# Kernel tuning notes

Measured on AMD Instinct MI355X. Metric: run time of the kernel, lower is better.

The kernel has to match this reference:

```python
import jax, jax.numpy as jnp
import numpy as np

H = 16  # num heads

def setup_inputs() -> dict:
    key = jax.random.key(0)
    ks = jax.random.split(key, 5)
    B, S, D = 4, 2048, 1024
    scale = 1.0 / np.sqrt(D)
    return {
        "hidden_states": jax.random.normal(ks[0], (B, S, D), dtype=jnp.float32),
        "Wq": jax.random.normal(ks[1], (D, D), dtype=jnp.float32) * scale,
        "Wk": jax.random.normal(ks[2], (D, D), dtype=jnp.float32) * scale,
        "Wv": jax.random.normal(ks[3], (D, D), dtype=jnp.float32) * scale,
        "Wo": jax.random.normal(ks[4], (D, D), dtype=jnp.float32) * scale,
    }

def reference(hidden_states, Wq, Wk, Wv, Wo):
    B, S, D = hidden_states.shape
    hd = D // H  # attention_head_size

    def split_heads(x):  # [B,S,D] -> [B,H,S,hd]
        return x.reshape(B, S, H, hd).transpose(0, 2, 1, 3)

    # torch Linear (no bias): y = x @ W.T
    q = split_heads(hidden_states @ Wq.T)
    k = split_heads(hidden_states @ Wk.T)
    v = split_heads(hidden_states @ Wv.T)

    scores = jnp.einsum('bhqd,bhkd->bhqk', q, k) / jnp.sqrt(jnp.float32(hd))
    probs = jax.nn.softmax(scores, axis=-1)  # dropout p=0 -> identity
    ctx = jnp.einsum('bhqk,bhkd->bhqd', probs, v)
    ctx = ctx.transpose(0, 2, 1, 3).reshape(B, S, D)
    out = ctx @ Wo.T
    return out
```

## Files before the change

### kernel.cpp

```cpp
#include <hip/hip_runtime.h>

typedef _Float16 half8 __attribute__((ext_vector_type(8)));
typedef _Float16 half4 __attribute__((ext_vector_type(4)));
typedef float f32x4 __attribute__((ext_vector_type(4)));

#define GLOAD16(gptr, lptr)                                                               \
  __builtin_amdgcn_global_load_lds((const __attribute__((address_space(1))) void*)(gptr), \
                                   (__attribute__((address_space(3))) void*)(lptr), 16, 0, 0)

#define MEMFENCE asm volatile("" ::: "memory")

constexpr int B_ = 4, S_ = 2048, D_ = 1024;
constexpr int M_ = B_ * S_;

__global__ __launch_bounds__(256) void cvt_all(
    const float* __restrict__ x, const float* __restrict__ wq,
    const float* __restrict__ wk, const float* __restrict__ wv,
    const float* __restrict__ wo, _Float16* __restrict__ xb,
    _Float16* __restrict__ wb ) {
  int bx = blockIdx.x;
  const float* src;
  _Float16* dst;
  long i;
  if (bx < 4096) {
    src = x; dst = xb; i = (long)bx * 256 + threadIdx.x;
  } else {
    int seg = (bx - 4096) >> 9;
    src = seg == 0 ? wq : seg == 1 ? wk : seg == 2 ? wv : wo;
    dst = wb + (long)seg * D_ * D_;
    i = (long)((bx - 4096) & 511) * 256 + threadIdx.x;
  }
  const float4* s4 = (const float4*)src;
  float4 a = s4[2 * i], b = s4[2 * i + 1];
  half8 o = {(_Float16)a.x, (_Float16)a.y, (_Float16)a.z, (_Float16)a.w,
             (_Float16)b.x, (_Float16)b.y, (_Float16)b.z, (_Float16)b.w};
  *(half8*)(dst + 8 * i) = o;
}

__device__ __forceinline__ void gemm_core(const _Float16* __restrict__ A,
                                          const _Float16* __restrict__ W,
                                          _Float16* As, _Float16* Bs, long m0,
                                          long n0, int t, f32x4 acc[4][4]) {
  const int lane = t & 63, w = t >> 6, wr = w >> 1, wc = w & 1;
  const int r16 = lane & 15, g = lane >> 4;
  const int srow = t >> 2, schunk = t & 3;
  const int sc = schunk ^ (srow & 3);
  const _Float16* Ap = A + (m0 + srow) * D_ + sc * 8;
  const _Float16* Wp = W + (n0 + srow) * D_ + sc * 8;
  _Float16* Ad = As + srow * 32 + schunk * 8;
  _Float16* Bd = Bs + srow * 32 + schunk * 8;
  for (int k0 = 0; k0 < D_; k0 += 32) {
    GLOAD16(Ap + k0, Ad);
    GLOAD16(Ap + 64 * D_ + k0, Ad + 64 * 32);
    GLOAD16(Wp + k0, Bd);
    GLOAD16(Wp + 64 * D_ + k0, Bd + 64 * 32);
    __syncthreads();
    half8 af[4], bf[4];
#pragma unroll
    for (int i = 0; i < 4; ++i) {
      int ra = wr * 64 + i * 16 + r16;
      int rb = wc * 64 + i * 16 + r16;
      af[i] = *(const half8*)(As + ra * 32 + ((g ^ (ra & 3)) * 8));
      bf[i] = *(const half8*)(Bs + rb * 32 + ((g ^ (rb & 3)) * 8));
    }
#pragma unroll
    for (int i = 0; i < 4; ++i)
#pragma unroll
      for (int j = 0; j < 4; ++j)
        acc[i][j] =
            __builtin_amdgcn_mfma_f32_16x16x32_f16(af[i], bf[j], acc[i][j], 0, 0, 0);
    __syncthreads();
  }
}

__global__ __launch_bounds__(256, 2) void gemm_qkv(
    const _Float16* __restrict__ A, const _Float16* __restrict__ Wq,
    const _Float16* __restrict__ Wk, const _Float16* __restrict__ Wv,
    _Float16* __restrict__ Qo, _Float16* __restrict__ Ko,
    _Float16* __restrict__ Vt) {
  __shared__ _Float16 As[128 * 32], Bs[128 * 32];
  const int t = threadIdx.x;
  const int sel = blockIdx.y >> 3;
  const _Float16* W = sel == 0 ? Wq : (sel == 1 ? Wk : Wv);
  long m0 = (long)blockIdx.x * 128;
  long n0 = (long)(blockIdx.y & 7) * 128;
  f32x4 acc[4][4] = {};
  gemm_core(A, W, As, Bs, m0, n0, t, acc);
  const int lane = t & 63, w = t >> 6, wr = w >> 1, wc = w & 1;
  const int r16 = lane & 15, g = lane >> 4;
  if (sel < 2) {
    _Float16* C = sel == 0 ? Qo : Ko;
#pragma unroll
    for (int i = 0; i < 4; ++i)
#pragma unroll
      for (int j = 0; j < 4; ++j)
#pragma unroll
        for (int r = 0; r < 4; ++r) {
          long mr = m0 + wr * 64 + i * 16 + g * 4 + r;
          long nc = n0 + wc * 64 + j * 16 + r16;
          C[mr * D_ + nc] = (_Float16)acc[i][j][r];
        }
  } else {
#pragma unroll
    for (int i = 0; i < 4; ++i)
#pragma unroll
      for (int j = 0; j < 4; ++j)
#pragma unroll
        for (int r = 0; r < 4; ++r) {
          long mr = m0 + wr * 64 + i * 16 + g * 4 + r;
          long nc = n0 + wc * 64 + j * 16 + r16;
          long bb = mr >> 11, ss = mr & 2047;
          long hh = nc >> 6, dd = nc & 63;
          Vt[(((bb * 16 + hh) * 64 + dd) << 11) + ss] = (_Float16)acc[i][j][r];
        }
  }
}

__global__ __launch_bounds__(256, 2) void gemm_out(const _Float16* __restrict__ A,
                                                   const _Float16* __restrict__ W,
                                                   float* __restrict__ C) {
  __shared__ _Float16 As[128 * 32], Bs[128 * 32];
  const int t = threadIdx.x;
  long m0 = (long)blockIdx.x * 128;
  long n0 = (long)blockIdx.y * 128;
  f32x4 acc[4][4] = {};
  gemm_core(A, W, As, Bs, m0, n0, t, acc);
  const int lane = t & 63, w = t >> 6, wr = w >> 1, wc = w & 1;
  const int r16 = lane & 15, g = lane >> 4;
#pragma unroll
  for (int i = 0; i < 4; ++i)
#pragma unroll
    for (int j = 0; j < 4; ++j)
#pragma unroll
      for (int r = 0; r < 4; ++r) {
        long mr = m0 + wr * 64 + i * 16 + g * 4 + r;
        long nc = n0 + wc * 64 + j * 16 + r16;
        C[mr * D_ + nc] = acc[i][j][r];
      }
}

__global__ __launch_bounds__(512, 4) void attn_kernel(
    const _Float16* __restrict__ Q, const _Float16* __restrict__ K,
    const _Float16* __restrict__ Vt, _Float16* __restrict__ Ctx) {
  __shared__ _Float16 Ks[2][64 * 64], Vs[2][64 * 64];
  const int t = threadIdx.x, lane = t & 63, w = t >> 6;
  const int r16 = lane & 15, g = lane >> 4;
  const int q0 = blockIdx.x * 256;
  const int bh = blockIdx.y;
  const int b = bh >> 4, h = bh & 15;
  const long qkbase = ((long)b * S_) * D_ + h * 64;
  const long vtbase = (long)bh * 64 * S_;

  half8 qf[2][2];
#pragma unroll
  for (int mi = 0; mi < 2; ++mi)
#pragma unroll
    for (int ks = 0; ks < 2; ++ks) {
      int row = q0 + w * 32 + mi * 16 + r16;
      half8 v = *(const half8*)(Q + qkbase + (long)row * D_ + ks * 32 + g * 8);
      qf[mi][ks] = v * (_Float16)0.125f;
    }
  asm volatile("s_waitcnt vmcnt(0)" ::: "memory");

  f32x4 ctx[2][4] = {};
  float lsum[2] = {0.f, 0.f};

  const int srowt = t >> 3, schunk = t & 7;
  const int sc = schunk ^ (srowt & 7);
  const _Float16* Kg = K + qkbase + (long)srowt * D_ + sc * 8;
  const _Float16* Vg = Vt + vtbase + (long)srowt * S_ + sc * 8;

#define STAGE(kt, buf)                                                  \
  do {                                                                  \
    GLOAD16(Kg + (long)(kt)*64 * D_, &Ks[buf][srowt * 64 + schunk * 8]); \
    GLOAD16(Vg + (kt)*64, &Vs[buf][srowt * 64 + schunk * 8]);            \
  } while (0)

  STAGE(0, 0);
  constexpr int NT = S_ / 64;
  for (int kt = 0; kt < NT; ++kt) {
    const int cur = kt & 1;
    if (kt + 1 < NT) {
      STAGE(kt + 1, cur ^ 1);
      asm volatile("s_waitcnt vmcnt(2)" ::: "memory");
    } else {
      asm volatile("s_waitcnt vmcnt(0)" ::: "memory");
    }
    __builtin_amdgcn_s_barrier();
    MEMFENCE;
    __builtin_amdgcn_sched_barrier(0);
    const _Float16* Kc = Ks[cur];
    const _Float16* Vc = Vs[cur];

    f32x4 sf[4][2] = {};
#pragma unroll
    for (int kn = 0; kn < 4; ++kn) {
#pragma unroll
      for (int ks = 0; ks < 2; ++ks) {
        int row = kn * 16 + r16;
        int ch = ks * 4 + g;
        half8 kf = *(const half8*)(Kc + row * 64 + ((ch ^ (row & 7)) * 8));
        sf[kn][0] = __builtin_amdgcn_mfma_f32_16x16x32_f16(kf, qf[0][ks], sf[kn][0], 0, 0, 0);
        sf[kn][1] = __builtin_amdgcn_mfma_f32_16x16x32_f16(kf, qf[1][ks], sf[kn][1], 0, 0, 0);
      }
    }

    half4 pt[4][2];
#pragma unroll
    for (int kn = 0; kn < 4; ++kn)
#pragma unroll
      for (int mi = 0; mi < 2; ++mi) {
        float p0 = __expf(sf[kn][mi][0]);
        float p1 = __expf(sf[kn][mi][1]);
        float p2 = __expf(sf[kn][mi][2]);
        float p3 = __expf(sf[kn][mi][3]);
        lsum[mi] += (p0 + p1) + (p2 + p3);
        half4 pk = {(_Float16)p0, (_Float16)p1, (_Float16)p2, (_Float16)p3};
        pt[kn][mi] = pk;
      }

#pragma unroll
    for (int ni = 0; ni < 4; ++ni) {
      int row = ni * 16 + r16;
#pragma unroll
      for (int kt16 = 0; kt16 < 4; ++kt16) {
        int ch = kt16 * 2 + (g >> 1);
        half4 vf = *(const half4*)(Vc + row * 64 + ((ch ^ (row & 7)) * 8) + (g & 1) * 4);
        ctx[0][ni] = __builtin_amdgcn_mfma_f32_16x16x16f16(pt[kt16][0], vf, ctx[0][ni], 0, 0, 0);
        ctx[1][ni] = __builtin_amdgcn_mfma_f32_16x16x16f16(pt[kt16][1], vf, ctx[1][ni], 0, 0, 0);
      }
    }
    __builtin_amdgcn_sched_barrier(0);
    asm volatile("s_waitcnt lgkmcnt(0)" ::: "memory");
    MEMFENCE;
    __builtin_amdgcn_s_barrier();
    MEMFENCE;
  }
#undef STAGE

  float linv[2];
#pragma unroll
  for (int mi = 0; mi < 2; ++mi) {
    float v = lsum[mi];
    v += __shfl_xor(v, 16);
    v += __shfl_xor(v, 32);
    linv[mi] = 1.f / v;
  }
#pragma unroll
  for (int mi = 0; mi < 2; ++mi)
#pragma unroll
    for (int r = 0; r < 4; ++r) {
      float inv = __shfl(linv[mi], g * 4 + r, 16);
      long qrow = (long)b * S_ + q0 + w * 32 + mi * 16 + g * 4 + r;
#pragma unroll
      for (int ni = 0; ni < 4; ++ni)
        Ctx[qrow * D_ + h * 64 + ni * 16 + r16] = (_Float16)(ctx[mi][ni][r] * inv);
    }
}

extern "C" void kernel_launch(void* const* d_in, const int* in_sizes, int n_in,
                              void* d_out, int out_size, void* d_ws, size_t ws_size,
                              hipStream_t stream) {
  (void)in_sizes; (void)n_in; (void)out_size; (void)ws_size;
  const float* x = (const float*)d_in[0];
  const float* Wq = (const float*)d_in[1];
  const float* Wk = (const float*)d_in[2];
  const float* Wv = (const float*)d_in[3];
  const float* Wo = (const float*)d_in[4];
  char* ws = (char*)d_ws;
  _Float16* xb = (_Float16*)ws;
  _Float16* wb = (_Float16*)(ws + (size_t)16 * 1024 * 1024);
  _Float16* wqb = wb;
  _Float16* wkb = wb + (size_t)D_ * D_;
  _Float16* wvb = wb + (size_t)2 * D_ * D_;
  _Float16* wob = wb + (size_t)3 * D_ * D_;
  _Float16* qb = (_Float16*)(ws + (size_t)24 * 1024 * 1024);
  _Float16* kb = qb + (size_t)M_ * D_;
  _Float16* vtb = kb + (size_t)M_ * D_;
  _Float16* ctxb = vtb + (size_t)M_ * D_;

  cvt_all<<<4096 + 4 * 512, 256, 0, stream>>>(x, Wq, Wk, Wv, Wo, xb, wb);
  gemm_qkv<<<dim3(64, 24), 256, 0, stream>>>(xb, wqb, wkb, wvb, qb, kb, vtb);
  attn_kernel<<<dim3(8, 64), 512, 0, stream>>>(qb, kb, vtb, ctxb);
  gemm_out<<<dim3(64, 8), 256, 0, stream>>>(ctxb, wob, (float*)d_out);
}
```

Baseline: 202.0 us.

## Fold softmax scale and log2e into Q projection, permute Vt for 16-byte LDS reads

The 1/sqrt(hd)·log2(e) factor is now applied in the QKV GEMM epilogue, so the attention kernel drops its per-fragment Q multiply and calls exp2f instead of __expf. The V-transpose store permutes the sequence index within each 64-block so the PV loop can load one half8 per LDS read and split it into two half4 MFMA operands, halving the number of LDS reads for V. This saves exp-argument scaling and LDS instructions in the inner loop, at the cost of extra index arithmetic in the V store epilogue and a layout the two kernels must agree on.

```diff
diff --git a/kernel.cpp b/kernel.cpp
--- a/kernel.cpp
+++ b/kernel.cpp
@@ -12,6 +12,7 @@
 
 constexpr int B_ = 4, S_ = 2048, D_ = 1024;
 constexpr int M_ = B_ * S_;
+#define QSCALE 0.18033688f
 
 __global__ __launch_bounds__(256) void cvt_all(
     const float* __restrict__ x, const float* __restrict__ wq,
@@ -90,6 +91,7 @@
   const int r16 = lane & 15, g = lane >> 4;
   if (sel < 2) {
     _Float16* C = sel == 0 ? Qo : Ko;
+    const float qs = sel == 0 ? QSCALE : 1.0f;
 #pragma unroll
     for (int i = 0; i < 4; ++i)
 #pragma unroll
@@ -98,7 +100,7 @@
         for (int r = 0; r < 4; ++r) {
           long mr = m0 + wr * 64 + i * 16 + g * 4 + r;
           long nc = n0 + wc * 64 + j * 16 + r16;
-          C[mr * D_ + nc] = (_Float16)acc[i][j][r];
+          C[mr * D_ + nc] = (_Float16)(acc[i][j][r] * qs);
         }
   } else {
 #pragma unroll
@@ -110,8 +112,11 @@
           long mr = m0 + wr * 64 + i * 16 + g * 4 + r;
           long nc = n0 + wc * 64 + j * 16 + r16;
           long bb = mr >> 11, ss = mr & 2047;
+          int s6 = (int)(ss & 63);
+          int sp = ((s6 >> 2) & 3) * 16 + (s6 >> 5) * 8 + ((s6 >> 4) & 1) * 4 + (s6 & 3);
+          long ssp = (ss & ~63L) | sp;
           long hh = nc >> 6, dd = nc & 63;
-          Vt[(((bb * 16 + hh) * 64 + dd) << 11) + ss] = (_Float16)acc[i][j][r];
+          Vt[(((bb * 16 + hh) * 64 + dd) << 11) + ssp] = (_Float16)acc[i][j][r];
         }
   }
 }
@@ -157,8 +162,7 @@
 #pragma unroll
     for (int ks = 0; ks < 2; ++ks) {
       int row = q0 + w * 32 + mi * 16 + r16;
-      half8 v = *(const half8*)(Q + qkbase + (long)row * D_ + ks * 32 + g * 8);
-      qf[mi][ks] = v * (_Float16)0.125f;
+      qf[mi][ks] = *(const half8*)(Q + qkbase + (long)row * D_ + ks * 32 + g * 8);
     }
   asm volatile("s_waitcnt vmcnt(0)" ::: "memory");
 
@@ -210,10 +214,10 @@
     for (int kn = 0; kn < 4; ++kn)
 #pragma unroll
       for (int mi = 0; mi < 2; ++mi) {
-        float p0 = __expf(sf[kn][mi][0]);
-        float p1 = __expf(sf[kn][mi][1]);
-        float p2 = __expf(sf[kn][mi][2]);
-        float p3 = __expf(sf[kn][mi][3]);
+        float p0 = exp2f(sf[kn][mi][0]);
+        float p1 = exp2f(sf[kn][mi][1]);
+        float p2 = exp2f(sf[kn][mi][2]);
+        float p3 = exp2f(sf[kn][mi][3]);
         lsum[mi] += (p0 + p1) + (p2 + p3);
         half4 pk = {(_Float16)p0, (_Float16)p1, (_Float16)p2, (_Float16)p3};
         pt[kn][mi] = pk;
@@ -223,11 +227,15 @@
     for (int ni = 0; ni < 4; ++ni) {
       int row = ni * 16 + r16;
 #pragma unroll
-      for (int kt16 = 0; kt16 < 4; ++kt16) {
-        int ch = kt16 * 2 + (g >> 1);
-        half4 vf = *(const half4*)(Vc + row * 64 + ((ch ^ (row & 7)) * 8) + (g & 1) * 4);
-        ctx[0][ni] = __builtin_amdgcn_mfma_f32_16x16x16f16(pt[kt16][0], vf, ctx[0][ni], 0, 0, 0);
-        ctx[1][ni] = __builtin_amdgcn_mfma_f32_16x16x16f16(pt[kt16][1], vf, ctx[1][ni], 0, 0, 0);
+      for (int j2 = 0; j2 < 2; ++j2) {
+        int ch = g * 2 + j2;
+        half8 vf8 = *(const half8*)(Vc + row * 64 + ((ch ^ (row & 7)) * 8));
+        half4 v0 = __builtin_shufflevector(vf8, vf8, 0, 1, 2, 3);
+        half4 v1 = __builtin_shufflevector(vf8, vf8, 4, 5, 6, 7);
+        ctx[0][ni] = __builtin_amdgcn_mfma_f32_16x16x16f16(pt[2 * j2][0], v0, ctx[0][ni], 0, 0, 0);
+        ctx[1][ni] = __builtin_amdgcn_mfma_f32_16x16x16f16(pt[2 * j2][1], v0, ctx[1][ni], 0, 0, 0);
+        ctx[0][ni] = __builtin_amdgcn_mfma_f32_16x16x16f16(pt[2 * j2 + 1][0], v1, ctx[0][ni], 0, 0, 0);
+        ctx[1][ni] = __builtin_amdgcn_mfma_f32_16x16x16f16(pt[2 * j2 + 1][1], v1, ctx[1][ni], 0, 0, 0);
       }
     }
     __builtin_amdgcn_sched_barrier(0);
```

New measurement: 216.4 us. 7.1% more time.
